# Optimization experiments

Hardware: AMD Instinct MI355X
Metric: run time of the kernel (lower is better)

Reference implementation:

```python
import jax, jax.numpy as jnp
import numpy as np

N_KNOTS = 16
DEGREE = 3
EPS = 1e-8


def make_knots(n_knots, degree):
    knots = np.zeros(n_knots, dtype=np.float32)
    for i in range(n_knots):
        if i <= degree:
            knots[i] = 0.0
        elif i >= n_knots - degree - 1:
            knots[i] = 1.0
        else:
            knots[i] = (i - degree) / (n_knots - 2 * degree - 1)
    return knots


def setup_inputs() -> dict:
    key = jax.random.key(0)
    k1, k2 = jax.random.split(key)
    x = jax.random.uniform(k1, (65536, 64), dtype=jnp.float32)
    control_points = jax.random.normal(k2, (64, 12, 64), dtype=jnp.float32)
    return {"x": x, "control_points": control_points}


def bspline_basis(x, knots_np, degree):
    # x: [B, D] in [0,1]; returns basis: [B, D, n_control_points]
    n_knots = knots_np.shape[0]
    n_intervals = n_knots - 1
    knots = jnp.asarray(knots_np)
    xe = x[..., None]  # [B, D, 1]
    left = knots[:-1]
    right = knots[1:]
    in_interval = (xe >= left) & (xe < right)
    last = (xe >= left[-1]) & (xe <= right[-1])  # include right endpoint of last interval
    basis = jnp.concatenate([in_interval[..., :-1], last], axis=-1).astype(x.dtype)
    for k in range(1, degree + 1):
        nb = n_intervals - k
        j = np.arange(nb)
        dL = knots_np[j + k] - knots_np[j]          # constants
        dR = knots_np[j + k + 1] - knots_np[j + 1]
        okL = np.abs(dL) > EPS
        okR = np.abs(dR) > EPS
        invL = jnp.asarray(np.where(okL, 1.0 / np.where(okL, dL, 1.0), 0.0).astype(np.float32))
        invR = jnp.asarray(np.where(okR, 1.0 / np.where(okR, dR, 1.0), 0.0).astype(np.float32))
        cL = (xe - knots[j]) * invL                 # [B, D, nb], zero where degenerate
        cR = (knots[j + k + 1] - xe) * invR
        basis = cL * basis[..., :nb] + cR * basis[..., 1:nb + 1]
    return basis


def reference(x, control_points):
    # x: [B, in_dim]; control_points: [in_dim, n_cp, out_dim]
    knots_np = make_knots(N_KNOTS, DEGREE)
    xc = jnp.clip(x, 0.0, 1.0)
    basis = bspline_basis(xc, knots_np, DEGREE)     # [B, in_dim, n_cp]
    return jnp.einsum('bic,ico->bo', basis, control_points)
```

## Files before the change

kernel.cpp:

```cpp
#include <hip/hip_runtime.h>


typedef short short8 __attribute__((ext_vector_type(8)));
typedef float f32x4 __attribute__((ext_vector_type(4)));
typedef unsigned u32x4 __attribute__((ext_vector_type(4)));
typedef unsigned long long u64;

#define THREADS 256

static __device__ __forceinline__ unsigned bf16rne(float f) {
  unsigned u = __float_as_uint(f);
  return (u + 0x7FFFu + ((u >> 16) & 1u)) >> 16;
}

__global__ __launch_bounds__(256) void prep_wfrag(const float* __restrict__ cp,
                                                  unsigned* __restrict__ wfrag) {
  int id = blockIdx.x * 256 + threadIdx.x;
  int d  = id & 3;
  int l  = (id >> 2) & 63;
  int id2 = id >> 8;
  int nt = id2 / 24;
  int s  = id2 - nt * 24;
  int g  = l >> 4;
  int o  = nt * 16 + (l & 15);
  int k0 = 192 * g + 8 * s + 2 * d;
  unsigned lo = bf16rne(cp[k0 * 64 + o]);
  unsigned hi = bf16rne(cp[(k0 + 1) * 64 + o]);
  wfrag[id] = lo | (hi << 16);
}

static __device__ __forceinline__ void eval_chunks(float xi, u64& c0, u64& c1, u64& c2) {
  xi = fminf(fmaxf(xi, 0.0f), 1.0f);
  float t9 = xi * 9.0f;
  int jj = (int)t9;
  float validf = (jj <= 8) ? 1.0f : 0.0f;
  jj = (jj > 8) ? 8 : jj;
  float fj = (float)jj;
  float u  = t9 - fj;
  float omu = 1.0f - u;
  float k1c = fminf(fj, 1.0f);
  float k2c = fminf(fj, 2.0f);
  float rdj = 9.0f - fj;
  float d2p = fminf(rdj, 2.0f);
  float d3p = fminf(rdj, 3.0f);
  float invA = (jj == 0) ? 1.0f : 0.5f;
  float invB = (jj == 8) ? 1.0f : 0.5f;
  float invC = (jj == 0) ? 1.0f : ((jj == 1) ? 0.5f : (1.0f / 3.0f));
  float invD = (jj == 0 || jj == 8) ? 0.5f : (1.0f / 3.0f);
  float invE = (jj >= 7) ? ((jj == 8) ? 1.0f : 0.5f) : (1.0f / 3.0f);
  float xkm1 = u + k1c, xkm2 = u + k2c;
  float k2x = d2p - u, k3x = d3p - u;
  float t0 = omu * invA;
  float A0 = omu * t0;
  float s1 = xkm1 * t0;
  float t1 = u * invB;
  float A1 = fmaf(k2x, t1, s1);
  float A2 = u * t1;
  float u0 = A0 * invC;
  float B0 = omu * u0;
  float s2 = xkm2 * u0;
  float u1 = A1 * invD;
  float B1 = fmaf(k2x, u1, s2);
  float s3 = xkm1 * u1;
  float u2 = A2 * invE;
  float B2 = fmaf(k3x, u2, s3);
  float B3 = u * u2;
  B0 *= validf; B1 *= validf; B2 *= validf; B3 *= validf;

  unsigned lo = bf16rne(B0) | (bf16rne(B1) << 16);
  unsigned hi = bf16rne(B2) | (bf16rne(B3) << 16);
  u64 P = (u64)lo | ((u64)hi << 32);
  int s0 = jj << 4;
  c0 = (s0 < 64) ? (P << (s0 & 63)) : 0ull;
  c1 = (s0 < 64) ? ((s0 == 0) ? 0ull : (P >> ((64 - s0) & 63)))
                 : ((s0 < 128) ? (P << ((s0 - 64) & 63)) : 0ull);
  c2 = (s0 > 64) ? (P >> ((128 - s0) & 63)) : 0ull;
}

static __device__ __forceinline__ short8 mk_frag(u64 lo64, u64 hi64) {
  u32x4 q = { (unsigned)lo64, (unsigned)(lo64 >> 32),
              (unsigned)hi64, (unsigned)(hi64 >> 32) };
  return __builtin_bit_cast(short8, q);
}

__global__ __launch_bounds__(THREADS, 4) void kan_mfma(const float* __restrict__ x,
                                                       const unsigned* __restrict__ wfrag,
                                                       float* __restrict__ out) {
  const int tid  = threadIdx.x;
  const int lane = tid & 63;
  const int w    = tid >> 6;
  const int m = lane & 15, g = lane >> 4;
  const long row0 = (long)blockIdx.x * 64 + w * 16;

  float xr[16];
  {
    const float4* p0 = (const float4*)(x + (row0 + m) * 64 + g * 16);
    #pragma unroll
    for (int q = 0; q < 4; ++q) {
      float4 v = p0[q];
      xr[4 * q] = v.x; xr[4 * q + 1] = v.y; xr[4 * q + 2] = v.z; xr[4 * q + 3] = v.w;
    }
  }

  f32x4 acc[4];
  #pragma unroll
  for (int nt = 0; nt < 4; ++nt) acc[nt] = f32x4{0.0f, 0.0f, 0.0f, 0.0f};

  const u32x4* wf4 = (const u32x4*)wfrag;

  #pragma unroll
  for (int q = 0; q < 8; ++q) {
    u32x4 bq[4][3];
    #pragma unroll
    for (int nt = 0; nt < 4; ++nt)
      #pragma unroll
      for (int sub = 0; sub < 3; ++sub)
        bq[nt][sub] = wf4[(nt * 24 + 3 * q + sub) * 64 + lane];

    u64 a0, a1, a2, b0, b1, b2;
    eval_chunks(xr[2 * q],     a0, a1, a2);
    eval_chunks(xr[2 * q + 1], b0, b1, b2);

    short8 A[3] = { mk_frag(a0, a1), mk_frag(a2, b0), mk_frag(b1, b2) };

    #pragma unroll
    for (int sub = 0; sub < 3; ++sub)
      #pragma unroll
      for (int nt = 0; nt < 4; ++nt)
        acc[nt] = __builtin_amdgcn_mfma_f32_16x16x32_bf16(
            A[sub], __builtin_bit_cast(short8, bq[nt][sub]), acc[nt], 0, 0, 0);
  }

  #pragma unroll
  for (int nt = 0; nt < 4; ++nt)
    #pragma unroll
    for (int j = 0; j < 4; ++j)
      out[(row0 + g * 4 + j) * 64 + nt * 16 + m] = acc[nt][j];
}

extern "C" void kernel_launch(void* const* d_in, const int* in_sizes, int n_in,
                              void* d_out, int out_size, void* d_ws, size_t ws_size,
                              hipStream_t stream) {
  const float* x  = (const float*)d_in[0];
  const float* cp = (const float*)d_in[1];
  float* out = (float*)d_out;
  unsigned* wfrag = (unsigned*)d_ws;

  hipLaunchKernelGGL(prep_wfrag, dim3(96), dim3(256), 0, stream, cp, wfrag);
  const int rows = in_sizes[0] / 64;
  hipLaunchKernelGGL(kan_mfma, dim3(rows / 64), dim3(THREADS), 0, stream,
                     x, wfrag, out);
}
```

Measured before the change: 84.78 us.

## Split K across wave pairs, give each wave two M tiles, reduce via LDS

Each block now handles 128 rows with 8 waves. Each wave computes two 16-row M tiles so that every loaded B fragment feeds two MFMAs, and the K dimension (input features) is split between two wave halves. Partial sums from the second half are written to shared memory and added by the first half before the store. This halves B-fragment global loads per MFMA, but it adds an LDS reduction, a block barrier, and about 34KB of shared memory per block, which may limit occupancy.

Result: faster. 81.73 us (-3.6%).

```diff
diff --git a/kernel.cpp b/kernel.cpp
--- a/kernel.cpp
+++ b/kernel.cpp
@@ -6,7 +6,7 @@
 typedef unsigned u32x4 __attribute__((ext_vector_type(4)));
 typedef unsigned long long u64;
 
-#define THREADS 256
+#define THREADS 512
 
 static __device__ __forceinline__ unsigned bf16rne(float f) {
   unsigned u = __float_as_uint(f);
@@ -86,56 +86,109 @@
 __global__ __launch_bounds__(THREADS, 4) void kan_mfma(const float* __restrict__ x,
                                                        const unsigned* __restrict__ wfrag,
                                                        float* __restrict__ out) {
+  __shared__ float red[4 * 64 * 33];
   const int tid  = threadIdx.x;
   const int lane = tid & 63;
   const int w    = tid >> 6;
+  const int kh   = w >> 2;
+  const int rt   = w & 3;
   const int m = lane & 15, g = lane >> 4;
-  const long row0 = (long)blockIdx.x * 64 + w * 16;
-
-  float xr[16];
+  const long row0 = (long)blockIdx.x * 128 + rt * 32;
+
+  float xr0[8], xr1[8];
   {
-    const float4* p0 = (const float4*)(x + (row0 + m) * 64 + g * 16);
-    #pragma unroll
-    for (int q = 0; q < 4; ++q) {
+    const float4* p0 = (const float4*)(x + (row0 + m) * 64 + g * 16 + kh * 8);
+    const float4* p1 = (const float4*)(x + (row0 + 16 + m) * 64 + g * 16 + kh * 8);
+    #pragma unroll
+    for (int q = 0; q < 2; ++q) {
       float4 v = p0[q];
-      xr[4 * q] = v.x; xr[4 * q + 1] = v.y; xr[4 * q + 2] = v.z; xr[4 * q + 3] = v.w;
+      xr0[4 * q] = v.x; xr0[4 * q + 1] = v.y; xr0[4 * q + 2] = v.z; xr0[4 * q + 3] = v.w;
+      float4 v1 = p1[q];
+      xr1[4 * q] = v1.x; xr1[4 * q + 1] = v1.y; xr1[4 * q + 2] = v1.z; xr1[4 * q + 3] = v1.w;
     }
   }
 
-  f32x4 acc[4];
+  f32x4 acc[2][4];
   #pragma unroll
-  for (int nt = 0; nt < 4; ++nt) acc[nt] = f32x4{0.0f, 0.0f, 0.0f, 0.0f};
+  for (int mt = 0; mt < 2; ++mt)
+    #pragma unroll
+    for (int nt = 0; nt < 4; ++nt)
+      acc[mt][nt] = f32x4{0.0f, 0.0f, 0.0f, 0.0f};
 
   const u32x4* wf4 = (const u32x4*)wfrag;
 
   #pragma unroll
-  for (int q = 0; q < 8; ++q) {
-    u32x4 bq[4][3];
-    #pragma unroll
-    for (int nt = 0; nt < 4; ++nt)
+  for (int q = 0; q < 4; ++q) {
+    const int sbase = kh * 12 + 3 * q;
+
+    u32x4 b01[2][3];
+    #pragma unroll
+    for (int nt = 0; nt < 2; ++nt)
       #pragma unroll
       for (int sub = 0; sub < 3; ++sub)
-        bq[nt][sub] = wf4[(nt * 24 + 3 * q + sub) * 64 + lane];
+        b01[nt][sub] = wf4[(nt * 24 + sbase + sub) * 64 + lane];
 
     u64 a0, a1, a2, b0, b1, b2;
-    eval_chunks(xr[2 * q],     a0, a1, a2);
-    eval_chunks(xr[2 * q + 1], b0, b1, b2);
-
-    short8 A[3] = { mk_frag(a0, a1), mk_frag(a2, b0), mk_frag(b1, b2) };
+    eval_chunks(xr0[2 * q],     a0, a1, a2);
+    eval_chunks(xr0[2 * q + 1], b0, b1, b2);
+    short8 A0[3] = { mk_frag(a0, a1), mk_frag(a2, b0), mk_frag(b1, b2) };
+    eval_chunks(xr1[2 * q],     a0, a1, a2);
+    eval_chunks(xr1[2 * q + 1], b0, b1, b2);
+    short8 A1[3] = { mk_frag(a0, a1), mk_frag(a2, b0), mk_frag(b1, b2) };
 
     #pragma unroll
     for (int sub = 0; sub < 3; ++sub)
       #pragma unroll
+      for (int nt = 0; nt < 2; ++nt) {
+        short8 B = __builtin_bit_cast(short8, b01[nt][sub]);
+        acc[0][nt] = __builtin_amdgcn_mfma_f32_16x16x32_bf16(A0[sub], B, acc[0][nt], 0, 0, 0);
+        acc[1][nt] = __builtin_amdgcn_mfma_f32_16x16x32_bf16(A1[sub], B, acc[1][nt], 0, 0, 0);
+      }
+
+    u32x4 b23[2][3];
+    #pragma unroll
+    for (int nt = 0; nt < 2; ++nt)
+      #pragma unroll
+      for (int sub = 0; sub < 3; ++sub)
+        b23[nt][sub] = wf4[((nt + 2) * 24 + sbase + sub) * 64 + lane];
+
+    #pragma unroll
+    for (int sub = 0; sub < 3; ++sub)
+      #pragma unroll
+      for (int nt = 0; nt < 2; ++nt) {
+        short8 B = __builtin_bit_cast(short8, b23[nt][sub]);
+        acc[0][nt + 2] = __builtin_amdgcn_mfma_f32_16x16x32_bf16(A0[sub], B, acc[0][nt + 2], 0, 0, 0);
+        acc[1][nt + 2] = __builtin_amdgcn_mfma_f32_16x16x32_bf16(A1[sub], B, acc[1][nt + 2], 0, 0, 0);
+      }
+  }
+
+  const int rbase = (rt * 64 + lane) * 33;
+  if (kh == 1) {
+    #pragma unroll
+    for (int mt = 0; mt < 2; ++mt)
+      #pragma unroll
       for (int nt = 0; nt < 4; ++nt)
-        acc[nt] = __builtin_amdgcn_mfma_f32_16x16x32_bf16(
-            A[sub], __builtin_bit_cast(short8, bq[nt][sub]), acc[nt], 0, 0, 0);
-  }
-
-  #pragma unroll
-  for (int nt = 0; nt < 4; ++nt)
-    #pragma unroll
-    for (int j = 0; j < 4; ++j)
-      out[(row0 + g * 4 + j) * 64 + nt * 16 + m] = acc[nt][j];
+        #pragma unroll
+        for (int j = 0; j < 4; ++j)
+          red[rbase + mt * 16 + nt * 4 + j] = acc[mt][nt][j];
+  }
+  __syncthreads();
+  if (kh == 0) {
+    #pragma unroll
+    for (int mt = 0; mt < 2; ++mt)
+      #pragma unroll
+      for (int nt = 0; nt < 4; ++nt)
+        #pragma unroll
+        for (int j = 0; j < 4; ++j)
+          acc[mt][nt][j] += red[rbase + mt * 16 + nt * 4 + j];
+    #pragma unroll
+    for (int mt = 0; mt < 2; ++mt)
+      #pragma unroll
+      for (int nt = 0; nt < 4; ++nt)
+        #pragma unroll
+        for (int j = 0; j < 4; ++j)
+          out[(row0 + mt * 16 + g * 4 + j) * 64 + nt * 16 + m] = acc[mt][nt][j];
+  }
 }
 
 extern "C" void kernel_launch(void* const* d_in, const int* in_sizes, int n_in,
@@ -148,6 +201,6 @@
 
   hipLaunchKernelGGL(prep_wfrag, dim3(96), dim3(256), 0, stream, cp, wfrag);
   const int rows = in_sizes[0] / 64;
-  hipLaunchKernelGGL(kan_mfma, dim3(rows / 64), dim3(THREADS), 0, stream,
+  hipLaunchKernelGGL(kan_mfma, dim3(rows / 128), dim3(THREADS), 0, stream,
                      x, wfrag, out);
 }
```
